# Kernel optimization log

Measured on AMD Instinct MI355X. Metric: run time of the kernel, lower is better.

Reference implementation:

```python
import jax, jax.numpy as jnp
import numpy as np

EPS = 1e-5

def layer_norm(x, w, b):
    # normalize over last two dims [N, H]
    mean = jnp.mean(x, axis=(-2, -1), keepdims=True)
    var = jnp.var(x, axis=(-2, -1), keepdims=True)
    return (x - mean) * jax.lax.rsqrt(var + EPS) * w + b

def lg_conv(x, edge_index, num_nodes):
    # LightGCN conv: symmetric-normalized neighbor sum (no self loops)
    src, dst = edge_index[0], edge_index[1]
    deg = jnp.zeros((num_nodes,), x.dtype).at[dst].add(1.0)
    dinv = jnp.where(deg > 0, jax.lax.rsqrt(jnp.maximum(deg, 1.0)), 0.0)
    norm = dinv[src] * dinv[dst]                      # [E]
    msgs = x[:, :, src, :] * norm[None, None, :, None]  # [B,P,E,H]
    return jnp.zeros_like(x).at[:, :, dst, :].add(msgs)

def setup_inputs() -> dict:
    key = jax.random.key(0)
    ks = jax.random.split(key, 4)
    B, P, N, H = 16, 12, 2048, 64
    E = 16384
    x = jax.random.normal(ks[0], (B, P, N, H), dtype=jnp.float32)
    edge_index = jax.random.randint(ks[1], (2, E), 0, N, dtype=jnp.int64)
    g_norm_w = jnp.ones((N, H), jnp.float32)
    g_norm_b = jnp.zeros((N, H), jnp.float32)
    t_norm_w = jnp.ones((N, H), jnp.float32)
    t_norm_b = jnp.zeros((N, H), jnp.float32)
    bound = 1.0 / np.sqrt(P)  # Conv2d default init range
    conv_w = jax.random.uniform(ks[2], (P, P), jnp.float32, -bound, bound)
    conv_b = jax.random.uniform(ks[3], (P,), jnp.float32, -bound, bound)
    return {"x": x, "edge_index": edge_index,
            "g_norm_w": g_norm_w, "g_norm_b": g_norm_b,
            "t_norm_w": t_norm_w, "t_norm_b": t_norm_b,
            "conv_w": conv_w, "conv_b": conv_b}

def reference(x, edge_index, g_norm_w, g_norm_b, t_norm_w, t_norm_b, conv_w, conv_b):
    N = x.shape[2]
    h = layer_norm(x, g_norm_w, g_norm_b)
    h = lg_conv(h, edge_index, N)
    h = layer_norm(h, t_norm_w, t_norm_b)
    # 1x1 Conv2d over channels = periods: [B,P,N,H] -> [B,Q,N,H]
    out = jnp.einsum('qp,bpnh->bqnh', conv_w, h) + conv_b[None, :, None, None]
    return out
```

## Files before the change

### kernel.cpp

```cpp
#include <hip/hip_runtime.h>

#define B_ 16
#define P_ 12
#define N_ 2048
#define H_ 64
#define E_ 16384
#define NH_ (N_*H_)
#define NG_ (B_*P_)

#define WS_MEAN1  0
#define WS_RSTD1  192
#define WS_PA     384
#define WS_AG     2048
#define WS_BG     133120
#define WS_PC     264192
#define WS_ROWPTR 313344
#define WS_PAIR   315400

__global__ __launch_bounds__(1024) void k_stats_csr(const float* __restrict__ x,
                                                    const int* __restrict__ ew,
                                                    float* __restrict__ pA,
                                                    int* __restrict__ rowPtr,
                                                    int2* __restrict__ pair) {
    __shared__ int   sDeg[N_];
    __shared__ int   sA[N_];
    __shared__ int   sB[N_];
    __shared__ float sDinv[N_];
    __shared__ int   sFlag;
    __shared__ float ls[16], lq[16];
    int tid = threadIdx.x;
    if (blockIdx.x < 768) {
        int g = blockIdx.x >> 2, seg = blockIdx.x & 3;
        const float4* xg = (const float4*)(x + (size_t)g * NH_);
        float s = 0.f, q = 0.f;
        int base = seg * 8192;
        #pragma unroll
        for (int i = 0; i < 8; ++i) {
            float4 v = xg[base + i*1024 + tid];
            s += v.x + v.y + v.z + v.w;
            q += v.x*v.x + v.y*v.y + v.z*v.z + v.w*v.w;
        }
        for (int off = 32; off; off >>= 1) { s += __shfl_down(s, off); q += __shfl_down(q, off); }
        int wid = tid >> 6, lane = tid & 63;
        if (!lane) { ls[wid] = s; lq[wid] = q; }
        __syncthreads();
        if (!tid) {
            float S = 0.f, Q = 0.f;
            #pragma unroll
            for (int i = 0; i < 16; ++i) { S += ls[i]; Q += lq[i]; }
            pA[blockIdx.x*2]   = S;
            pA[blockIdx.x*2+1] = Q;
        }
        return;
    }
    if (!tid) sFlag = 1;
    for (int i = tid; i < N_; i += 1024) sDeg[i] = 0;
    __syncthreads();
    if (tid < 256) { if (ew[2*tid+1] != 0) atomicAnd(&sFlag, 0); }
    __syncthreads();
    int is64 = sFlag;
    for (int e = tid; e < E_; e += 1024) {
        int dst = is64 ? ew[2*(E_+e)] : ew[E_+e];
        atomicAdd(&sDeg[dst], 1);
    }
    __syncthreads();
    for (int i = tid; i < N_; i += 1024) {
        int d = sDeg[i];
        sDinv[i] = d > 0 ? rsqrtf((float)d) : 0.f;
        sA[i] = d;
    }
    __syncthreads();
    int* in = sA; int* out = sB;
    for (int st = 1; st < N_; st <<= 1) {
        for (int i = tid; i < N_; i += 1024) {
            int v = in[i];
            if (i >= st) v += in[i-st];
            out[i] = v;
        }
        __syncthreads();
        int* t = in; in = out; out = t;
    }
    for (int i = tid; i < N_; i += 1024) {
        int excl = in[i] - sDeg[i];
        rowPtr[i] = excl;
        out[i] = excl;
    }
    if (!tid) rowPtr[N_] = E_;
    __syncthreads();
    for (int e = tid; e < E_; e += 1024) {
        int src = is64 ? ew[2*e]       : ew[e];
        int dst = is64 ? ew[2*(E_+e)]  : ew[E_+e];
        int pos = atomicAdd(&out[dst], 1);
        int2 pr; pr.x = src; pr.y = __float_as_int(sDinv[src] * sDinv[dst]);
        pair[pos] = pr;
    }
}

__global__ __launch_bounds__(256) void k_ab(const float* __restrict__ gw,
                                            const float* __restrict__ gb,
                                            const int* __restrict__ rowPtr,
                                            const int2* __restrict__ pair,
                                            const float* __restrict__ pA,
                                            float* __restrict__ Ag,
                                            float* __restrict__ Bg,
                                            float* __restrict__ mean1,
                                            float* __restrict__ rstd1) {
    int tid = threadIdx.x;
    if (blockIdx.x == 512) {
        if (tid < NG_) {
            float s = 0.f, q = 0.f;
            #pragma unroll
            for (int i = 0; i < 4; ++i) {
                s += pA[(tid*4+i)*2];
                q += pA[(tid*4+i)*2+1];
            }
            float m = s * (1.0f/NH_);
            float v = q * (1.0f/NH_) - m*m;
            mean1[tid] = m;
            rstd1[tid] = rsqrtf(v + 1e-5f);
        }
        return;
    }
    int wid = tid >> 6, lane = tid & 63;
    int n = blockIdx.x*4 + wid;
    int j = rowPtr[n], e = rowPtr[n+1];
    float A = 0.f, Bv = 0.f;
    for (; j < e; ++j) {
        int2 pr = pair[j];
        float w = __int_as_float(pr.y);
        int ro = pr.x*H_ + lane;
        A  += w * gb[ro];
        Bv += w * gw[ro];
    }
    Ag[n*H_ + lane] = A;
    Bg[n*H_ + lane] = Bv;
}

__global__ __launch_bounds__(256) void k_gather(const float* __restrict__ x,
                                                const float* __restrict__ mean1,
                                                const float* __restrict__ rstd1,
                                                const int* __restrict__ rowPtr,
                                                const int2* __restrict__ pair,
                                                const float* __restrict__ Ag,
                                                const float* __restrict__ Bg,
                                                float* __restrict__ h2,
                                                float* __restrict__ pC) {
    int b     = blockIdx.x & 15;
    int chunk = blockIdx.x >> 4;
    int wid = threadIdx.x >> 6, lane = threadIdx.x & 63;
    __shared__ float s_rs[P_], s_mrs[P_];
    __shared__ float red[4][P_][2];
    if (threadIdx.x < P_) {
        float m = mean1[b*P_ + threadIdx.x], r = rstd1[b*P_ + threadIdx.x];
        s_rs[threadIdx.x] = r; s_mrs[threadIdx.x] = m*r;
    }
    __syncthreads();
    const float* xb = x + (size_t)b * P_ * NH_;
    int n0 = chunk*16 + wid*4;
    int r0 = rowPtr[n0], r1 = rowPtr[n0+1], r2 = rowPtr[n0+2],
        r3 = rowPtr[n0+3], r4 = rowPtr[n0+4];
    int j0 = r0, e0 = r1, j1 = r1, e1 = r2, j2 = r2, e2 = r3, j3 = r3, e3 = r4;
    float A0 = Ag[(n0+0)*H_+lane], B0 = Bg[(n0+0)*H_+lane];
    float A1 = Ag[(n0+1)*H_+lane], B1 = Bg[(n0+1)*H_+lane];
    float A2 = Ag[(n0+2)*H_+lane], B2 = Bg[(n0+2)*H_+lane];
    float A3 = Ag[(n0+3)*H_+lane], B3 = Bg[(n0+3)*H_+lane];
    float ac0[P_], ac1[P_], ac2[P_], ac3[P_];
    #pragma unroll
    for (int p = 0; p < P_; ++p) { ac0[p]=0.f; ac1[p]=0.f; ac2[p]=0.f; ac3[p]=0.f; }
    while ((j0 < e0) | (j1 < e1) | (j2 < e2) | (j3 < e3)) {
        if (j0 < e0) {
            int2 pr = pair[j0++]; float w = __int_as_float(pr.y); int ro = pr.x*H_ + lane;
            #pragma unroll
            for (int p = 0; p < P_; ++p) ac0[p] += w * xb[(size_t)p*NH_ + ro];
        }
        if (j1 < e1) {
            int2 pr = pair[j1++]; float w = __int_as_float(pr.y); int ro = pr.x*H_ + lane;
            #pragma unroll
            for (int p = 0; p < P_; ++p) ac1[p] += w * xb[(size_t)p*NH_ + ro];
        }
        if (j2 < e2) {
            int2 pr = pair[j2++]; float w = __int_as_float(pr.y); int ro = pr.x*H_ + lane;
            #pragma unroll
            for (int p = 0; p < P_; ++p) ac2[p] += w * xb[(size_t)p*NH_ + ro];
        }
        if (j3 < e3) {
            int2 pr = pair[j3++]; float w = __int_as_float(pr.y); int ro = pr.x*H_ + lane;
            #pragma unroll
            for (int p = 0; p < P_; ++p) ac3[p] += w * xb[(size_t)p*NH_ + ro];
        }
    }
    float sp[P_], qp[P_];
    #pragma unroll
    for (int p = 0; p < P_; ++p) { sp[p] = 0.f; qp[p] = 0.f; }
    size_t obb = (size_t)b*P_*NH_ + (size_t)n0*H_ + lane;
    #pragma unroll
    for (int p = 0; p < P_; ++p) {
        size_t op = obb + (size_t)p*NH_;
        float v0 = s_rs[p]*ac0[p] - s_mrs[p]*B0 + A0;
        float v1 = s_rs[p]*ac1[p] - s_mrs[p]*B1 + A1;
        float v2 = s_rs[p]*ac2[p] - s_mrs[p]*B2 + A2;
        float v3 = s_rs[p]*ac3[p] - s_mrs[p]*B3 + A3;
        h2[op]        = v0;
        h2[op + H_]   = v1;
        h2[op + 2*H_] = v2;
        h2[op + 3*H_] = v3;
        sp[p] += v0+v1+v2+v3;
        qp[p] += v0*v0+v1*v1+v2*v2+v3*v3;
    }
    #pragma unroll
    for (int p = 0; p < P_; ++p) {
        float s = sp[p], q = qp[p];
        for (int off = 32; off; off >>= 1) { s += __shfl_down(s, off); q += __shfl_down(q, off); }
        if (!lane) { red[wid][p][0] = s; red[wid][p][1] = q; }
    }
    __syncthreads();
    if (threadIdx.x < P_*2) {
        int p = threadIdx.x >> 1, c = threadIdx.x & 1;
        float v = red[0][p][c] + red[1][p][c] + red[2][p][c] + red[3][p][c];
        pC[(((b*P_ + p) << 7) + chunk)*2 + c] = v;
    }
}

__global__ __launch_bounds__(256) void k_mix(float* __restrict__ h2,
                                             const float* __restrict__ tw,
                                             const float* __restrict__ tb,
                                             const float* __restrict__ cw,
                                             const float* __restrict__ cb,
                                             const float* __restrict__ pC) {
    __shared__ float scw[P_*P_], scb[P_], sm[P_], sr[P_], srow[P_];
    int b     = blockIdx.x >> 7;
    int chunk = blockIdx.x & 127;
    int tid   = threadIdx.x;
    int wid   = tid >> 6, lane = tid & 63;
    if (tid < P_*P_) scw[tid] = cw[tid];
    if (tid < P_) scb[tid] = cb[tid];
    #pragma unroll
    for (int pp = 0; pp < 3; ++pp) {
        int p = wid*3 + pp;
        int g = b*P_ + p;
        float s = pC[((g<<7) + lane)*2]     + pC[((g<<7) + 64 + lane)*2];
        float q = pC[((g<<7) + lane)*2 + 1] + pC[((g<<7) + 64 + lane)*2 + 1];
        for (int off = 32; off; off >>= 1) { s += __shfl_down(s, off); q += __shfl_down(q, off); }
        if (!lane) {
            float m = s * (1.0f/NH_);
            sm[p] = m;
            sr[p] = rsqrtf(q * (1.0f/NH_) - m*m + 1e-5f);
        }
    }
    __syncthreads();
    if (tid < P_) {
        float rs = 0.f;
        #pragma unroll
        for (int p = 0; p < P_; ++p) rs += scw[tid*P_ + p];
        srow[tid] = rs;
    }
    __syncthreads();
    int elem4 = chunk*256 + tid;
    size_t base = (size_t)b * P_ * NH_;
    float4 v[P_];
    #pragma unroll
    for (int p = 0; p < P_; ++p) {
        float4 t = *(const float4*)(h2 + base + (size_t)p*NH_ + (size_t)elem4*4);
        float m = sm[p], r = sr[p];
        v[p].x = (t.x-m)*r; v[p].y = (t.y-m)*r; v[p].z = (t.z-m)*r; v[p].w = (t.w-m)*r;
    }
    float4 tw4 = *(const float4*)(tw + (size_t)elem4*4);
    float4 tb4 = *(const float4*)(tb + (size_t)elem4*4);
    #pragma unroll
    for (int q = 0; q < P_; ++q) {
        float4 a = {0.f,0.f,0.f,0.f};
        #pragma unroll
        for (int p = 0; p < P_; ++p) {
            float c = scw[q*P_ + p];
            a.x += c*v[p].x; a.y += c*v[p].y; a.z += c*v[p].z; a.w += c*v[p].w;
        }
        float rb = srow[q], cbq = scb[q];
        float4 o;
        o.x = tw4.x*a.x + tb4.x*rb + cbq;
        o.y = tw4.y*a.y + tb4.y*rb + cbq;
        o.z = tw4.z*a.z + tb4.z*rb + cbq;
        o.w = tw4.w*a.w + tb4.w*rb + cbq;
        *(float4*)(h2 + base + (size_t)q*NH_ + (size_t)elem4*4) = o;
    }
}

extern "C" void kernel_launch(void* const* d_in, const int* in_sizes, int n_in,
                              void* d_out, int out_size, void* d_ws, size_t ws_size,
                              hipStream_t stream) {
    const float* x  = (const float*)d_in[0];
    const int*   ew = (const int*)d_in[1];
    const float* gw = (const float*)d_in[2];
    const float* gb = (const float*)d_in[3];
    const float* tw = (const float*)d_in[4];
    const float* tb = (const float*)d_in[5];
    const float* cw = (const float*)d_in[6];
    const float* cb = (const float*)d_in[7];
    float* out = (float*)d_out;
    float* wf  = (float*)d_ws;

    float* mean1  = wf + WS_MEAN1;
    float* rstd1  = wf + WS_RSTD1;
    float* pA     = wf + WS_PA;
    float* Ag     = wf + WS_AG;
    float* Bg     = wf + WS_BG;
    float* pC     = wf + WS_PC;
    int*   rowPtr = (int*)(wf + WS_ROWPTR);
    int2*  pair   = (int2*)(wf + WS_PAIR);

    k_stats_csr<<<769, 1024, 0, stream>>>(x, ew, pA, rowPtr, pair);
    k_ab<<<513, 256, 0, stream>>>(gw, gb, rowPtr, pair, pA, Ag, Bg, mean1, rstd1);
    k_gather<<<2048, 256, 0, stream>>>(x, mean1, rstd1, rowPtr, pair, Ag, Bg, out, pC);
    k_mix<<<2048, 256, 0, stream>>>(out, tw, tb, cw, cb, pC);
}
```

Before: 379.8 us.

## Remap gather threads to float4 over H with periods split across lane groups

In the gather kernel, each wave is now split into four 16-lane groups. Each group handles three of the twelve periods, and each lane loads a float4 of four H values. Nodes are processed one at a time instead of with four interleaved edge loops. The goal is wider vectorized loads, fewer scalar loads and fewer accumulator registers, and less divergence from the interleaved while-loop. The trade-off is less memory-level parallelism, since neighbor loads for different destination nodes no longer overlap, and each load instruction touches three scattered period planes.

```diff
diff --git a/kernel.cpp b/kernel.cpp
--- a/kernel.cpp
+++ b/kernel.cpp
@@ -147,75 +147,72 @@
                                                 float* __restrict__ pC) {
     int b     = blockIdx.x & 15;
     int chunk = blockIdx.x >> 4;
-    int wid = threadIdx.x >> 6, lane = threadIdx.x & 63;
+    int tid   = threadIdx.x;
+    int wid   = tid >> 6, lane = tid & 63;
+    int q     = lane >> 4, k = lane & 15;
     __shared__ float s_rs[P_], s_mrs[P_];
     __shared__ float red[4][P_][2];
-    if (threadIdx.x < P_) {
-        float m = mean1[b*P_ + threadIdx.x], r = rstd1[b*P_ + threadIdx.x];
-        s_rs[threadIdx.x] = r; s_mrs[threadIdx.x] = m*r;
-    }
-    __syncthreads();
-    const float* xb = x + (size_t)b * P_ * NH_;
-    int n0 = chunk*16 + wid*4;
-    int r0 = rowPtr[n0], r1 = rowPtr[n0+1], r2 = rowPtr[n0+2],
-        r3 = rowPtr[n0+3], r4 = rowPtr[n0+4];
-    int j0 = r0, e0 = r1, j1 = r1, e1 = r2, j2 = r2, e2 = r3, j3 = r3, e3 = r4;
-    float A0 = Ag[(n0+0)*H_+lane], B0 = Bg[(n0+0)*H_+lane];
-    float A1 = Ag[(n0+1)*H_+lane], B1 = Bg[(n0+1)*H_+lane];
-    float A2 = Ag[(n0+2)*H_+lane], B2 = Bg[(n0+2)*H_+lane];
-    float A3 = Ag[(n0+3)*H_+lane], B3 = Bg[(n0+3)*H_+lane];
-    float ac0[P_], ac1[P_], ac2[P_], ac3[P_];
-    #pragma unroll
-    for (int p = 0; p < P_; ++p) { ac0[p]=0.f; ac1[p]=0.f; ac2[p]=0.f; ac3[p]=0.f; }
-    while ((j0 < e0) | (j1 < e1) | (j2 < e2) | (j3 < e3)) {
-        if (j0 < e0) {
-            int2 pr = pair[j0++]; float w = __int_as_float(pr.y); int ro = pr.x*H_ + lane;
-            #pragma unroll
-            for (int p = 0; p < P_; ++p) ac0[p] += w * xb[(size_t)p*NH_ + ro];
-        }
-        if (j1 < e1) {
-            int2 pr = pair[j1++]; float w = __int_as_float(pr.y); int ro = pr.x*H_ + lane;
-            #pragma unroll
-            for (int p = 0; p < P_; ++p) ac1[p] += w * xb[(size_t)p*NH_ + ro];
-        }
-        if (j2 < e2) {
-            int2 pr = pair[j2++]; float w = __int_as_float(pr.y); int ro = pr.x*H_ + lane;
-            #pragma unroll
-            for (int p = 0; p < P_; ++p) ac2[p] += w * xb[(size_t)p*NH_ + ro];
-        }
-        if (j3 < e3) {
-            int2 pr = pair[j3++]; float w = __int_as_float(pr.y); int ro = pr.x*H_ + lane;
-            #pragma unroll
-            for (int p = 0; p < P_; ++p) ac3[p] += w * xb[(size_t)p*NH_ + ro];
-        }
-    }
-    float sp[P_], qp[P_];
-    #pragma unroll
-    for (int p = 0; p < P_; ++p) { sp[p] = 0.f; qp[p] = 0.f; }
-    size_t obb = (size_t)b*P_*NH_ + (size_t)n0*H_ + lane;
-    #pragma unroll
-    for (int p = 0; p < P_; ++p) {
-        size_t op = obb + (size_t)p*NH_;
-        float v0 = s_rs[p]*ac0[p] - s_mrs[p]*B0 + A0;
-        float v1 = s_rs[p]*ac1[p] - s_mrs[p]*B1 + A1;
-        float v2 = s_rs[p]*ac2[p] - s_mrs[p]*B2 + A2;
-        float v3 = s_rs[p]*ac3[p] - s_mrs[p]*B3 + A3;
-        h2[op]        = v0;
-        h2[op + H_]   = v1;
-        h2[op + 2*H_] = v2;
-        h2[op + 3*H_] = v3;
-        sp[p] += v0+v1+v2+v3;
-        qp[p] += v0*v0+v1*v1+v2*v2+v3*v3;
-    }
-    #pragma unroll
-    for (int p = 0; p < P_; ++p) {
-        float s = sp[p], q = qp[p];
-        for (int off = 32; off; off >>= 1) { s += __shfl_down(s, off); q += __shfl_down(q, off); }
-        if (!lane) { red[wid][p][0] = s; red[wid][p][1] = q; }
-    }
-    __syncthreads();
-    if (threadIdx.x < P_*2) {
-        int p = threadIdx.x >> 1, c = threadIdx.x & 1;
+    if (tid < P_) {
+        float m = mean1[b*P_ + tid], r = rstd1[b*P_ + tid];
+        s_rs[tid] = r; s_mrs[tid] = m*r;
+    }
+    __syncthreads();
+    float rs0 = s_rs[q],  rs1 = s_rs[q+4],  rs2 = s_rs[q+8];
+    float ms0 = s_mrs[q], ms1 = s_mrs[q+4], ms2 = s_mrs[q+8];
+    const float* xb  = x + (size_t)b * P_ * NH_;
+    const float* xp0 = xb + (size_t)q     * NH_;
+    const float* xp1 = xb + (size_t)(q+4) * NH_;
+    const float* xp2 = xb + (size_t)(q+8) * NH_;
+    int hh = k*4;
+    float sp0=0.f, sp1=0.f, sp2=0.f, qp0=0.f, qp1=0.f, qp2=0.f;
+    #pragma unroll
+    for (int i = 0; i < 4; ++i) {
+        int n  = chunk*16 + wid*4 + i;
+        int r0 = rowPtr[n], r1 = rowPtr[n+1];
+        float4 a0 = {0,0,0,0}, a1 = {0,0,0,0}, a2 = {0,0,0,0};
+        #pragma unroll 2
+        for (int j = r0; j < r1; ++j) {
+            int2 pr = pair[j];
+            float w = __int_as_float(pr.y);
+            int ro = pr.x*H_ + hh;
+            float4 x0 = *(const float4*)(xp0 + ro);
+            float4 x1 = *(const float4*)(xp1 + ro);
+            float4 x2 = *(const float4*)(xp2 + ro);
+            a0.x += w*x0.x; a0.y += w*x0.y; a0.z += w*x0.z; a0.w += w*x0.w;
+            a1.x += w*x1.x; a1.y += w*x1.y; a1.z += w*x1.z; a1.w += w*x1.w;
+            a2.x += w*x2.x; a2.y += w*x2.y; a2.z += w*x2.z; a2.w += w*x2.w;
+        }
+        float4 A4 = *(const float4*)(Ag + n*H_ + hh);
+        float4 B4 = *(const float4*)(Bg + n*H_ + hh);
+        float4 v0, v1, v2;
+        v0.x = rs0*a0.x - ms0*B4.x + A4.x;  v0.y = rs0*a0.y - ms0*B4.y + A4.y;
+        v0.z = rs0*a0.z - ms0*B4.z + A4.z;  v0.w = rs0*a0.w - ms0*B4.w + A4.w;
+        v1.x = rs1*a1.x - ms1*B4.x + A4.x;  v1.y = rs1*a1.y - ms1*B4.y + A4.y;
+        v1.z = rs1*a1.z - ms1*B4.z + A4.z;  v1.w = rs1*a1.w - ms1*B4.w + A4.w;
+        v2.x = rs2*a2.x - ms2*B4.x + A4.x;  v2.y = rs2*a2.y - ms2*B4.y + A4.y;
+        v2.z = rs2*a2.z - ms2*B4.z + A4.z;  v2.w = rs2*a2.w - ms2*B4.w + A4.w;
+        size_t bn = (size_t)b*P_*NH_ + (size_t)n*H_ + hh;
+        *(float4*)(h2 + bn + (size_t)q    *NH_) = v0;
+        *(float4*)(h2 + bn + (size_t)(q+4)*NH_) = v1;
+        *(float4*)(h2 + bn + (size_t)(q+8)*NH_) = v2;
+        sp0 += v0.x+v0.y+v0.z+v0.w;  qp0 += v0.x*v0.x+v0.y*v0.y+v0.z*v0.z+v0.w*v0.w;
+        sp1 += v1.x+v1.y+v1.z+v1.w;  qp1 += v1.x*v1.x+v1.y*v1.y+v1.z*v1.z+v1.w*v1.w;
+        sp2 += v2.x+v2.y+v2.z+v2.w;  qp2 += v2.x*v2.x+v2.y*v2.y+v2.z*v2.z+v2.w*v2.w;
+    }
+    #pragma unroll
+    for (int off = 1; off < 16; off <<= 1) {
+        sp0 += __shfl_xor(sp0, off); qp0 += __shfl_xor(qp0, off);
+        sp1 += __shfl_xor(sp1, off); qp1 += __shfl_xor(qp1, off);
+        sp2 += __shfl_xor(sp2, off); qp2 += __shfl_xor(qp2, off);
+    }
+    if (k == 0) {
+        red[wid][q  ][0] = sp0; red[wid][q  ][1] = qp0;
+        red[wid][q+4][0] = sp1; red[wid][q+4][1] = qp1;
+        red[wid][q+8][0] = sp2; red[wid][q+8][1] = qp2;
+    }
+    __syncthreads();
+    if (tid < P_*2) {
+        int p = tid >> 1, c = tid & 1;
         float v = red[0][p][c] + red[1][p][c] + red[2][p][c] + red[3][p][c];
         pC[(((b*P_ + p) << 7) + chunk)*2 + c] = v;
     }
```

After: 343.1 us. -9.7%, faster.
